# Performance work log

Measured on AMD Instinct MI355X. Metric: run time of the kernel, lower is better.

The kernel has to match this reference:

```python
import jax, jax.numpy as jnp
import numpy as np

N_NODES = 50000
N_EDGES = 200000
N_GRAPH = 1024
H = 128          # hidden_channels
POS = 48         # pos_offset
NF = 256         # num_filters in SchNetInteraction
L = 5            # n_layers
NFF = 512
MAX_ITEM = 300


def ssp(v):
    # shifted softplus used by SchNet
    return jax.nn.softplus(v) - jnp.log(2.0)


def setup_inputs() -> dict:
    key = jax.random.key(0)
    ks = iter(jax.random.split(key, 40))
    s = 0.05
    inp = {}
    inp['x'] = jax.random.randint(next(ks), (N_NODES,), 0, MAX_ITEM)
    inp['edge_index'] = jax.random.randint(next(ks), (2, N_EDGES), 0, N_NODES)
    inp['edge_attr'] = jax.random.normal(next(ks), (N_EDGES, 4), jnp.float32)
    inp['batch'] = jnp.sort(jax.random.randint(next(ks), (N_NODES,), 0, N_GRAPH))
    inp['pos'] = jax.random.normal(next(ks), (N_NODES, 3), jnp.float32)
    # embedding / projection params
    vert = jax.random.normal(next(ks), (MAX_ITEM + 1, H - POS), jnp.float32) * s
    inp['vert_emb'] = vert.at[MAX_ITEM].set(0.0)  # padding_idx
    inp['pos_w'] = jax.random.normal(next(ks), (POS, 3), jnp.float32) * s
    inp['edge_w'] = jax.random.normal(next(ks), (H, 4), jnp.float32) * s
    # per-layer SchNetInteraction params (stacked over L)
    inp['filt_w1'] = jax.random.normal(next(ks), (L, NF, H), jnp.float32) * s
    inp['filt_b1'] = jnp.zeros((L, NF), jnp.float32)
    inp['filt_w2'] = jax.random.normal(next(ks), (L, NF, NF), jnp.float32) * s
    inp['filt_b2'] = jnp.zeros((L, NF), jnp.float32)
    inp['lin1_w'] = jax.random.normal(next(ks), (L, NF, H), jnp.float32) * s
    inp['lin2_w'] = jax.random.normal(next(ks), (L, H, NF), jnp.float32) * s
    inp['lin2_b'] = jnp.zeros((L, H), jnp.float32)
    inp['lin3_w'] = jax.random.normal(next(ks), (L, H, H), jnp.float32) * s
    inp['lin3_b'] = jnp.zeros((L, H), jnp.float32)
    # per-layer edge MLP: Linear(edge_ch + in_ch -> in_ch) + Tanh
    inp['em_w'] = jax.random.normal(next(ks), (L, H, 2 * H), jnp.float32) * s
    inp['em_b'] = jnp.zeros((L, H), jnp.float32)
    # head
    inp['head_w1'] = jax.random.normal(next(ks), (NFF, H), jnp.float32) * s
    inp['head_b1'] = jnp.zeros((NFF,), jnp.float32)
    inp['head_w2'] = jax.random.normal(next(ks), (1, NFF), jnp.float32) * s
    inp['head_b2'] = jnp.zeros((1,), jnp.float32)
    return inp


def _forward(x, edge_index, edge_attr, batch, pos, vert_emb, pos_w, edge_w,
             filt_w1, filt_b1, filt_w2, filt_b2, lin1_w, lin2_w, lin2_b,
             lin3_w, lin3_b, em_w, em_b, head_w1, head_b1, head_w2, head_b2):
    n = x.shape[0]
    src, dst = edge_index[0], edge_index[1]
    h = jnp.concatenate([vert_emb[x], pos @ pos_w.T], axis=-1)  # [N, H]
    ea = edge_attr @ edge_w.T                                    # [E, H]
    for i in range(L):
        # SchNetInteraction / CFConv: per-edge filter MLP, gather, scatter-sum
        W = ssp(ea @ filt_w1[i].T + filt_b1[i]) @ filt_w2[i].T + filt_b2[i]  # [E, NF]
        hj = (h @ lin1_w[i].T)[src]                                          # [E, NF]
        agg = jax.ops.segment_sum(hj * W, dst, num_segments=n)               # [N, NF]
        out = ssp(agg @ lin2_w[i].T + lin2_b[i]) @ lin3_w[i].T + lin3_b[i]   # [N, H]
        h = jax.nn.relu(out) + h  # relu + residual skip
        # edge MLP update (always active in ResGraphModule)
        ea = jnp.tanh(jnp.concatenate([ea, h[src] + h[dst]], axis=-1) @ em_w[i].T + em_b[i]) + ea
    # global mean pool over graphs
    ssum = jax.ops.segment_sum(h, batch, num_segments=N_GRAPH)               # [G, H]
    cnt = jax.ops.segment_sum(jnp.ones((n,), h.dtype), batch, num_segments=N_GRAPH)
    g = ssum / jnp.maximum(cnt, 1.0)[:, None]
    # head: Linear -> GELU (exact, as torch default) -> Dropout(eval) -> Linear
    y = jax.nn.gelu(g @ head_w1.T + head_b1, approximate=False) @ head_w2.T + head_b2
    return y  # [G, 1]


def reference(x, edge_index, edge_attr, batch, pos, vert_emb, pos_w, edge_w,
              filt_w1, filt_b1, filt_w2, filt_b2, lin1_w, lin2_w, lin2_b,
              lin3_w, lin3_b, em_w, em_b, head_w1, head_b1, head_w2, head_b2):
    return _forward(x, edge_index, edge_attr, batch, pos, vert_emb, pos_w, edge_w,
                    filt_w1, filt_b1, filt_w2, filt_b2, lin1_w, lin2_w, lin2_b,
                    lin3_w, lin3_b, em_w, em_b, head_w1, head_b1, head_w2, head_b2)
```

## Files before the change

### kernel.cpp

```cpp
#include <hip/hip_runtime.h>
#include <hip/hip_bf16.h>
#include <math.h>

#define N_NODES 50000
#define N_EDGES 200000
#define N_GRAPH 1024
#define HC      128
#define NFC     256
#define NLAYER  5
#define NFFC    512

typedef short bf16x8 __attribute__((ext_vector_type(8)));
typedef float f4v    __attribute__((ext_vector_type(4)));

__device__ __forceinline__ float ssp_f(float x) {
  float e = __expf(-fabsf(x));
  return fmaxf(x, 0.0f) + __logf(1.0f + e) - 0.69314718055994530942f;
}
__device__ __forceinline__ float tanh_f(float x) {
  float e = __expf(2.0f * fabsf(x));
  float t = 1.0f - 2.0f * __builtin_amdgcn_rcpf(e + 1.0f);
  return copysignf(t, x);
}
__device__ __forceinline__ unsigned short f2bf(float x) {
  union { float f; unsigned u; } v; v.f = x;
  unsigned r = v.u + 0x7fff + ((v.u >> 16) & 1);
  return (unsigned short)(r >> 16);
}
__device__ __forceinline__ float bf2f(unsigned short b) {
  union { unsigned u; float f; } v; v.u = (unsigned)b << 16; return v.f;
}

__global__ void zero_kernel(float4* __restrict__ p, int n4) {
  int i = blockIdx.x * blockDim.x + threadIdx.x;
  if (i < n4) p[i] = make_float4(0.f, 0.f, 0.f, 0.f);
}
__global__ void zeroi_kernel(int* __restrict__ p, int n) {
  int i = blockIdx.x * blockDim.x + threadIdx.x;
  if (i < n) p[i] = 0;
}

__global__ void hist_kernel(const int* __restrict__ ei, int* __restrict__ deg) {
  int e = blockIdx.x * blockDim.x + threadIdx.x;
  if (e < N_EDGES) atomicAdd(&deg[ei[N_EDGES + e]], 1);
}
__global__ void scan1_kernel(const int* __restrict__ deg, int* __restrict__ excl,
                             int* __restrict__ bsum, int n) {
  __shared__ int buf[256];
  const int tid = threadIdx.x;
  const int i = blockIdx.x * 256 + tid;
  int v = (i < n) ? deg[i] : 0;
  buf[tid] = v;
  __syncthreads();
  for (int s = 1; s < 256; s <<= 1) {
    int t = (tid >= s) ? buf[tid - s] : 0;
    __syncthreads();
    buf[tid] += t;
    __syncthreads();
  }
  if (i < n) excl[i] = buf[tid] - v;
  if (tid == 255) bsum[blockIdx.x] = buf[255];
}
__global__ void scan2_kernel(int* __restrict__ bsum, int nb) {
// ... 37 lines not shown

__global__ void wconv_kernel(const float* __restrict__ w,
                             unsigned short* __restrict__ hi, int n) {
  int i = blockIdx.x * blockDim.x + threadIdx.x;
  if (i < n) hi[i] = f2bf(w[i]);
}

__global__ void embed_kernel(const int* __restrict__ x, const float* __restrict__ pos,
                             const float* __restrict__ vert, const float* __restrict__ posw,
                             unsigned short* __restrict__ h) {
  int n = blockIdx.x;
  int c = threadIdx.x;
  float v;
  if (c < 80) {
    v = vert[(size_t)x[n] * 80 + c];
  } else {
    int j = c - 80;
    v = pos[n*3+0]*posw[j*3+0] + pos[n*3+1]*posw[j*3+1] + pos[n*3+2]*posw[j*3+2];
  }
  h[(size_t)n*HC + c] = f2bf(v);
}

__global__ void edgeproj_kernel(const float* __restrict__ eattr, const float* __restrict__ ew,
                                unsigned short* __restrict__ eaP,
                                const int* __restrict__ ipos) {
  int idx = blockIdx.x * blockDim.x + threadIdx.x;
  if (idx >= N_EDGES * HC) return;
  int e = idx >> 7, c = idx & 127;
  const float* a = eattr + (size_t)e*4;
  const float* w = ew + (size_t)c*4;
  eaP[(size_t)ipos[e]*HC + c] = f2bf(a[0]*w[0] + a[1]*w[1] + a[2]*w[2] + a[3]*w[3]);
}

__global__ __launch_bounds__(256, 4) void emlite_kernel(
    unsigned short* eaP,
    const unsigned short* __restrict__ Bh,
    const float* __restrict__ bias,
    const int* __restrict__ eiPs, const int* __restrict__ eiPd,
    const unsigned short* __restrict__ hfeat)
{
  __shared__ unsigned short ldsA[64][136];
  __shared__ unsigned short ldsH[64][136];

  const int tid  = threadIdx.x;
  const int m0   = blockIdx.x * 64;
  const int lane = tid & 63, wave = tid >> 6;
  const int quad = lane >> 4, l16 = lane & 15;
  const int r = tid >> 2, cb = (tid & 3) * 32;

  const int e = m0 + r;
  const int s = eiPs[e], d = eiPd[e];

  {
    const unsigned short* ap = eaP + (size_t)e * HC + cb;
#pragma unroll
    for (int q = 0; q < 4; q++)
      *(bf16x8*)&ldsA[r][cb + q*8] = *(const bf16x8*)(ap + q*8);
    const unsigned short* p1 = hfeat + (size_t)s * HC + cb;
    const unsigned short* p2 = hfeat + (size_t)d * HC + cb;
    unsigned short x1[32], x2[32], th[32];
#pragma unroll
    for (int q = 0; q < 4; q++) {
      *(bf16x8*)&x1[q*8] = *(const bf16x8*)(p1 + q*8);
      *(bf16x8*)&x2[q*8] = *(const bf16x8*)(p2 + q*8);
    }
#pragma unroll
    for (int j = 0; j < 32; j++) th[j] = f2bf(bf2f(x1[j]) + bf2f(x2[j]));
#pragma unroll
    for (int q = 0; q < 4; q++)
      *(bf16x8*)&ldsH[r][cb + q*8] = *(bf16x8*)&th[q*8];
  }

  const f4v zf = {0.f, 0.f, 0.f, 0.f};
  f4v acc[4][2];
#pragma unroll
  for (int mt = 0; mt < 4; mt++) { acc[mt][0] = zf; acc[mt][1] = zf; }

  __syncthreads();

#pragma unroll
  for (int nt = 0; nt < 2; nt++) {
    const size_t brow = (size_t)(wave*32 + nt*16 + l16);
#pragma unroll
    for (int kk = 0; kk < 128; kk += 32) {
      bf16x8 b = *(const bf16x8*)&Bh[brow * 2*HC + kk + quad*8];
#pragma unroll
      for (int mt = 0; mt < 4; mt++) {
        bf16x8 a = *(const bf16x8*)&ldsA[mt*16 + l16][kk + quad*8];
        acc[mt][nt] = __builtin_amdgcn_mfma_f32_16x16x32_bf16(a, b, acc[mt][nt], 0, 0, 0);
      }
    }
#pragma unroll
    for (int kk = 0; kk < 128; kk += 32) {
      bf16x8 b = *(const bf16x8*)&Bh[brow * 2*HC + HC + kk + quad*8];
#pragma unroll
      for (int mt = 0; mt < 4; mt++) {
        bf16x8 a = *(const bf16x8*)&ldsH[mt*16 + l16][kk + quad*8];
        acc[mt][nt] = __builtin_amdgcn_mfma_f32_16x16x32_bf16(a, b, acc[mt][nt], 0, 0, 0);
      }
    }
  }

#pragma unroll
  for (int nt = 0; nt < 2; nt++) {
    const int col = wave*32 + nt*16 + l16;
    const float bz = bias[col];
#pragma unroll
    for (int mt = 0; mt < 4; mt++) {
      const int rowb = mt*16 + quad*4;
#pragma unroll
      for (int rr = 0; rr < 4; rr++) {
        const size_t idx = (size_t)(m0 + rowb + rr) * HC + col;
        eaP[idx] = f2bf(tanh_f(acc[mt][nt][rr] + bz) + bf2f(ldsA[rowb + rr][col]));
      }
    }
  }
}

__global__ __launch_bounds__(256, 2) void nodeup_kernel(
    float* __restrict__ agg,
    const unsigned short* __restrict__ L2h,
    const float* __restrict__ b2,
    const unsigned short* __restrict__ L3h,
    const float* __restrict__ b3,
    unsigned short* h)
{
  __shared__ unsigned short lds[128 * 136];

  const int tid  = threadIdx.x;
  const int m0   = blockIdx.x * 128;
  const int lane = tid & 63, wave = tid >> 6;
  const int quad = lane >> 4, l16 = lane & 15;
  const int wm = (wave >> 1) * 64, wn = (wave & 1) * 64;
  const int r  = tid >> 1;
  const int c0 = (tid & 1) * 16;

  const f4v zf = {0.f, 0.f, 0.f, 0.f};
  f4v acc[4][4];
#pragma unroll
  for (int i = 0; i < 4; i++)
#pragma unroll
    for (int j = 0; j < 4; j++) acc[i][j] = zf;

  const bool mok = (m0 + r) < N_NODES;
  const size_t arow = (size_t)(m0 + r);

  float av[16];
  if (mok) {
    const float* ap = agg + arow * NFC + c0;
#pragma unroll
    for (int q = 0; q < 4; q++) *(float4*)&av[q*4] = *(const float4*)(ap + q*4);
  } else {
#pragma unroll
    for (int j = 0; j < 16; j++) av[j] = 0.f;
  }

  for (int kk = 0; kk < NFC; kk += 32) {
    float avn[16];
    if (kk + 32 < NFC) {
      if (mok) {
        const float* ap = agg + arow * NFC + kk + 32 + c0;
#pragma unroll
        for (int q = 0; q < 4; q++) *(float4*)&avn[q*4] = *(const float4*)(ap + q*4);
      } else {
#pragma unroll
        for (int j = 0; j < 16; j++) avn[j] = 0.f;
      }
    }
    bf16x8 b[4];
#pragma unroll
    for (int nt = 0; nt < 4; nt++) {
      const size_t brow = (size_t)(wn + nt*16 + l16);
      b[nt] = *(const bf16x8*)&L2h[brow * NFC + kk + quad*8];
    }
    __syncthreads();
    unsigned short th[16];
#pragma unroll
    for (int j = 0; j < 16; j++) th[j] = f2bf(av[j]);
    *(bf16x8*)&lds[r*40 + c0]     = *(bf16x8*)&th[0];
    *(bf16x8*)&lds[r*40 + c0 + 8] = *(bf16x8*)&th[8];
    __syncthreads();
    bf16x8 a[4];
#pragma unroll
    for (int t = 0; t < 4; t++)
      a[t] = *(const bf16x8*)&lds[(wm + t*16 + l16) * 40 + quad * 8];
#pragma unroll
    for (int mt = 0; mt < 4; mt++)
#pragma unroll
      for (int nt = 0; nt < 4; nt++)
        acc[mt][nt] = __builtin_amdgcn_mfma_f32_16x16x32_bf16(a[mt], b[nt], acc[mt][nt], 0, 0, 0);
    if (kk + 32 < NFC) {
#pragma unroll
      for (int j = 0; j < 16; j++) av[j] = avn[j];
    }
  }
  __syncthreads();

  if (mok) {
    float4* zp = (float4*)(agg + arow * NFC + (tid & 1) * 128);
    const float4 z4 = make_float4(0.f, 0.f, 0.f, 0.f);
#pragma unroll
    for (int q = 0; q < 32; q++) zp[q] = z4;
  }

#pragma unroll
  for (int nt = 0; nt < 4; nt++) {
    const int col = wn + nt*16 + l16;
    const float bz = b2[col];
#pragma unroll
    for (int mt = 0; mt < 4; mt++) {
      const int rowb = wm + mt*16 + quad*4;
#pragma unroll
      for (int rr = 0; rr < 4; rr++)
        lds[(rowb+rr)*136 + col] = f2bf(ssp_f(acc[mt][nt][rr] + bz));
    }
  }
  __syncthreads();

  f4v acc2[4][4];
#pragma unroll
  for (int i = 0; i < 4; i++)
#pragma unroll
    for (int j = 0; j < 4; j++) acc2[i][j] = zf;

  for (int kk = 0; kk < HC; kk += 32) {
    bf16x8 b[4];
#pragma unroll
    for (int nt = 0; nt < 4; nt++) {
      const size_t brow = (size_t)(wn + nt*16 + l16);
      b[nt] = *(const bf16x8*)&L3h[brow * HC + kk + quad*8];
    }
    bf16x8 a[4];
#pragma unroll
    for (int t = 0; t < 4; t++)
      a[t] = *(const bf16x8*)&lds[(wm + t*16 + l16) * 136 + kk + quad * 8];
#pragma unroll
    for (int mt = 0; mt < 4; mt++)
#pragma unroll
      for (int nt = 0; nt < 4; nt++)
        acc2[mt][nt] = __builtin_amdgcn_mfma_f32_16x16x32_bf16(a[mt], b[nt], acc2[mt][nt], 0, 0, 0);
  }

#pragma unroll
  for (int nt = 0; nt < 4; nt++) {
    const int ncol = wn + nt*16 + l16;
    const float bz = b3[ncol];
#pragma unroll
    for (int mt = 0; mt < 4; mt++) {
      const int mb = wm + mt*16 + quad*4;
#pragma unroll
      for (int rr = 0; rr < 4; rr++) {
        const int m = m0 + mb + rr;
        if (m < N_NODES) {
          const size_t idx = (size_t)m * HC + ncol;
          h[idx] = f2bf(fmaxf(acc2[mt][nt][rr] + bz, 0.f) + bf2f(h[idx]));
        }
      }
    }
  }
}

__device__ __forceinline__ int sigma_row(int r) {
  return ((r >> 2) & 3) * 16 + (r >> 4) * 4 + (r & 3);
}
__global__ __launch_bounds__(256, 3) void ffs_kernel(
    const unsigned short* __restrict__ eaP,
    const unsigned short* __restrict__ l1h,
    const unsigned short* __restrict__ fw1h,
    const float* __restrict__ fb1,
    const unsigned short* __restrict__ fw2h,
    const float* __restrict__ fb2,
    const int* __restrict__ eiPs, const int* __restrict__ eiPd,
    const unsigned short* __restrict__ hfeat, float* __restrict__ agg)
{
  __shared__ unsigned short ldsA[64][136];
  __shared__ unsigned short ldsB[64][136];
  __shared__ int sD[64];

  const int tid  = threadIdx.x;
  const int m0   = blockIdx.x * 64;
  const int lane = tid & 63, wave = tid >> 6;
  const int quad = lane >> 4, l16 = lane & 15;
  const int r = tid >> 2, cb = (tid & 3) * 32;
  const int sp = m0 + sigma_row(r);

  const int s = eiPs[sp];
  bf16x8 hreg[4];
  {
    const unsigned short* hp = hfeat + (size_t)s * HC + cb;
#pragma unroll
    for (int q = 0; q < 4; q++) hreg[q] = *(const bf16x8*)(hp + q*8);
  }
  if (tid < 64) sD[tid] = eiPd[m0 + sigma_row(tid)];

  {
    const unsigned short* ap = eaP + (size_t)sp * HC + cb;
#pragma unroll
    for (int q = 0; q < 4; q++)
      *(bf16x8*)&ldsA[r][cb + q*8] = *(const bf16x8*)(ap + q*8);
  }

  const f4v zf = {0.f, 0.f, 0.f, 0.f};
  f4v wacc[4][4];
#pragma unroll
  for (int mt = 0; mt < 4; mt++)
#pragma unroll
    for (int nt = 0; nt < 4; nt++) wacc[mt][nt] = zf;

  __syncthreads();

  for (int p = 0; p < 4; p++) {
    f4v tacc[4];
#pragma unroll
    for (int mt = 0; mt < 4; mt++) tacc[mt] = zf;
    const size_t b1row = (size_t)(p*64 + wave*16 + l16);
#pragma unroll
    for (int kk = 0; kk < 128; kk += 32) {
      bf16x8 b = *(const bf16x8*)&fw1h[b1row * HC + kk + quad*8];
#pragma unroll
      for (int mt = 0; mt < 4; mt++) {
        bf16x8 a = *(const bf16x8*)&ldsA[mt*16 + l16][kk + quad*8];
        tacc[mt] = __builtin_amdgcn_mfma_f32_16x16x32_bf16(a, b, tacc[mt], 0, 0, 0);
      }
    }
    {
      const int col = wave*16 + l16;
      const float bz = fb1[p*64 + col];
#pragma unroll
      for (int mt = 0; mt < 4; mt++) {
        const int rowb = mt*16 + quad*4;
#pragma unroll
        for (int rr = 0; rr < 4; rr++)
          ldsB[rowb+rr][col] = f2bf(ssp_f(tacc[mt][rr] + bz));
      }
    }
    __syncthreads();

#pragma unroll
    for (int kc = 0; kc < 2; kc++) {
      bf16x8 a_[4];
#pragma unroll
      for (int mt = 0; mt < 4; mt++)
        a_[mt] = *(const bf16x8*)&ldsB[mt*16 + l16][kc*32 + quad*8];
#pragma unroll
      for (int nt = 0; nt < 4; nt++) {
        const size_t brow = (size_t)(wave*64 + nt*16 + l16);
        bf16x8 b = *(const bf16x8*)&fw2h[brow * NFC + p*64 + kc*32 + quad*8];
#pragma unroll
        for (int mt = 0; mt < 4; mt++)
          wacc[mt][nt] = __builtin_amdgcn_mfma_f32_16x16x32_bf16(a_[mt], b, wacc[mt][nt], 0, 0, 0);
      }
    }
    __syncthreads();
  }

#pragma unroll
  for (int q = 0; q < 4; q++)
    *(bf16x8*)&ldsB[r][cb + q*8] = hreg[q];
  __syncthreads();

  f4v hacc[4][4];
#pragma unroll
  for (int mt = 0; mt < 4; mt++)
#pragma unroll
    for (int nt = 0; nt < 4; nt++) hacc[mt][nt] = zf;

#pragma unroll
  for (int kk = 0; kk < 128; kk += 32) {
    bf16x8 a_[4];
#pragma unroll
    for (int mt = 0; mt < 4; mt++)
      a_[mt] = *(const bf16x8*)&ldsB[mt*16 + l16][kk + quad*8];
#pragma unroll
    for (int nt = 0; nt < 4; nt++) {
      const size_t brow = (size_t)(wave*64 + nt*16 + l16);
      bf16x8 b = *(const bf16x8*)&l1h[brow * HC + kk + quad*8];
#pragma unroll
      for (int mt = 0; mt < 4; mt++)
        hacc[mt][nt] = __builtin_amdgcn_mfma_f32_16x16x32_bf16(a_[mt], b, hacc[mt][nt], 0, 0, 0);
    }
  }

#pragma unroll
  for (int nt = 0; nt < 4; nt++) {
    const int col = wave*64 + nt*16 + l16;
    const float bz = fb2[col];
    float accum = 0.f;
    int prev = -1;
    bool firstrun = true;
#pragma unroll
    for (int mt = 0; mt < 4; mt++) {
#pragma unroll
      for (int rr = 0; rr < 4; rr++) {
        const int prow = mt*16 + quad*4 + rr;
        const int d = sD[prow];
        const float v = (wacc[mt][nt][rr] + bz) * hacc[mt][nt][rr];
        if (d != prev) {
          if (prev >= 0) {
            if (firstrun) atomicAdd(&agg[(size_t)prev * NFC + col], accum);
            else          agg[(size_t)prev * NFC + col] = accum;
            firstrun = false;
          }
          accum = v; prev = d;
        } else {
          accum += v;
        }
      }
    }
    atomicAdd(&agg[(size_t)prev * NFC + col], accum);
  }
}

__global__ __launch_bounds__(256) void poolhead_kernel(
    const int* __restrict__ batch, const unsigned short* __restrict__ h,
    const float* __restrict__ w1, const float* __restrict__ b1,
    const float* __restrict__ w2, const float* __restrict__ b2,
    float* __restrict__ y)
{
  __shared__ float gs[HC];
  __shared__ float red[256];
  const int g = blockIdx.x;
  const int tid = threadIdx.x;

  int lo = 0, hi = N_NODES;
  while (lo < hi) { int m = (lo + hi) >> 1; if (batch[m] < g) lo = m + 1; else hi = m; }
  int lo2 = lo, hi2 = N_NODES;
  while (lo2 < hi2) { int m = (lo2 + hi2) >> 1; if (batch[m] < g + 1) lo2 = m + 1; else hi2 = m; }
  const int cnt = lo2 - lo;

  if (tid < HC) {
    float s = 0.f;
    for (int i = lo; i < lo2; i++) s += bf2f(h[(size_t)i * HC + tid]);
    gs[tid] = s / (float)max(cnt, 1);
  }
  __syncthreads();

  float partial = 0.f;
  for (int f = tid; f < NFFC; f += 256) {
    float acc = b1[f];
    const float* wr = w1 + (size_t)f * HC;
#pragma unroll 8
    for (int k = 0; k < HC; k++) acc = fmaf(gs[k], wr[k], acc);
// ... 56 lines not shown
  unsigned short* fw2h = (unsigned short*)alloc((size_t)n_fw2*2);
  unsigned short* l1h  = (unsigned short*)alloc((size_t)n_l1*2);
  unsigned short* l2h  = (unsigned short*)alloc((size_t)n_l2*2);
  unsigned short* l3h  = (unsigned short*)alloc((size_t)n_l3*2);
  unsigned short* emh  = (unsigned short*)alloc((size_t)n_em*2);

  const int NSCAN = N_NODES + 1;
  const int NB    = (NSCAN + 255) / 256;

  zeroi_kernel<<<(NSCAN+255)/256, 256, 0, stream>>>(deg, NSCAN);
  hist_kernel<<<(N_EDGES+255)/256, 256, 0, stream>>>(ei, deg);
  scan1_kernel<<<NB, 256, 0, stream>>>(deg, cursor, bsum, NSCAN);
  scan2_kernel<<<1, 256, 0, stream>>>(bsum, NB);
  scan3_kernel<<<NB, 256, 0, stream>>>(cursor, bsum, NSCAN);
  perm_kernel<<<(N_EDGES+255)/256, 256, 0, stream>>>(ei, cursor, perm);
  eperm_kernel<<<(N_EDGES+255)/256, 256, 0, stream>>>(ei, perm, eiPs, eiPd, ipos);

  wconv_kernel<<<(n_fw1+255)/256, 256, 0, stream>>>(fw1, fw1h, n_fw1);
  wconv_kernel<<<(n_fw2+255)/256, 256, 0, stream>>>(fw2, fw2h, n_fw2);
  wconv_kernel<<<(n_l1 +255)/256, 256, 0, stream>>>(l1w, l1h, n_l1);
  wconv_kernel<<<(n_l2 +255)/256, 256, 0, stream>>>(l2w, l2h, n_l2);
  wconv_kernel<<<(n_l3 +255)/256, 256, 0, stream>>>(l3w, l3h, n_l3);
  wconv_kernel<<<(n_em +255)/256, 256, 0, stream>>>(emw, emh, n_em);

  const int GN   = (N_NODES + 127) / 128;
  const int GE64 = N_EDGES / 64;

  embed_kernel<<<N_NODES, 128, 0, stream>>>(x, pos, vert, posw, h);
  edgeproj_kernel<<<(N_EDGES*HC + 255)/256, 256, 0, stream>>>(eattr, edgew, eaP, ipos);
  zero_kernel<<<((N_NODES*NFC/4) + 255)/256, 256, 0, stream>>>(
      (float4*)agg, N_NODES*NFC/4);

  for (int i = 0; i < NLAYER; ++i) {
    ffs_kernel<<<GE64, 256, 0, stream>>>(
        eaP, l1h + (size_t)i*NFC*HC,
        fw1h + (size_t)i*NFC*HC, fb1 + (size_t)i*NFC,
        fw2h + (size_t)i*NFC*NFC, fb2 + (size_t)i*NFC,
        eiPs, eiPd, h, agg);
    nodeup_kernel<<<GN, 256, 0, stream>>>(
        agg, l2h + (size_t)i*HC*NFC, l2b + (size_t)i*HC,
        l3h + (size_t)i*HC*HC, l3b + (size_t)i*HC, h);
    if (i < NLAYER - 1) {
      emlite_kernel<<<GE64, 256, 0, stream>>>(
          eaP, emh + (size_t)i*HC*2*HC, emb + (size_t)i*HC,
          eiPs, eiPd, h);
    }
  }

  poolhead_kernel<<<N_GRAPH, 256, 0, stream>>>(batch, h, hw1, hb1, hw2, hb2, out);
}
```

Before: 1.492 ms.

## Fuse edge-MLP update into filter kernel and double-buffer filter stages

Folds the per-layer edge MLP (tanh update of edge features) into the start of the next layer's filter/message kernel, reusing the already-loaded edge tile and source-node features so the edge features stay in shared memory rather than taking an extra global round trip and launch. The filter network's two-stage loop is unrolled with double-buffered LDS tiles, which removes one barrier per stage and overlaps the next first-layer GEMM with the second-layer consume. The node-update kernel now converts the whole aggregate row to bf16 in LDS up front instead of streaming it in chunks with two barriers per step. This costs more LDS and register pressure in the fused kernel and adds a runtime branch for the first layer.

```diff
diff --git a/kernel.cpp b/kernel.cpp
--- a/kernel.cpp
+++ b/kernel.cpp
@@ -132,249 +132,70 @@
   eaP[(size_t)ipos[e]*HC + c] = f2bf(a[0]*w[0] + a[1]*w[1] + a[2]*w[2] + a[3]*w[3]);
 }
 
-__global__ __launch_bounds__(256, 4) void emlite_kernel(
+__device__ __forceinline__ int sigma_row(int r) {
+  return ((r >> 2) & 3) * 16 + (r >> 4) * 4 + (r & 3);
+}
+
+#define TACC_COMPUTE(TDST, P)                                                   \
+  {                                                                             \
+    _Pragma("unroll")                                                           \
+    for (int mt_ = 0; mt_ < 4; mt_++) TDST[mt_] = zf;                           \
+    const size_t b1row_ = (size_t)((P)*64 + wave*16 + l16);                     \
+    _Pragma("unroll")                                                           \
+    for (int kk_ = 0; kk_ < 128; kk_ += 32) {                                   \
+      bf16x8 b_ = *(const bf16x8*)&fw1h[b1row_ * HC + kk_ + quad*8];            \
+      _Pragma("unroll")                                                         \
+      for (int mt_ = 0; mt_ < 4; mt_++) {                                       \
+        bf16x8 a_ = *(const bf16x8*)&ldsA[mt_*16 + l16][kk_ + quad*8];          \
+        TDST[mt_] = __builtin_amdgcn_mfma_f32_16x16x32_bf16(a_, b_, TDST[mt_], 0, 0, 0); \
+      }                                                                         \
+    }                                                                           \
+  }
+
+#define TWRITE(TSRC, BUF, P)                                                    \
+  {                                                                             \
+    const int col_ = wave*16 + l16;                                             \
+    const float bz_ = fb1[(P)*64 + col_];                                       \
+    _Pragma("unroll")                                                           \
+    for (int mt_ = 0; mt_ < 4; mt_++) {                                         \
+      const int rowb_ = mt_*16 + quad*4;                                        \
+      _Pragma("unroll")                                                         \
+      for (int rr_ = 0; rr_ < 4; rr_++)                                         \
+        ldsT[BUF][rowb_+rr_][col_] = f2bf(ssp_f(TSRC[mt_][rr_] + bz_));         \
+    }                                                                           \
+  }
+
+#define WCONSUME(BUF, P)                                                        \
+  {                                                                             \
+    _Pragma("unroll")                                                           \
+    for (int kc_ = 0; kc_ < 2; kc_++) {                                         \
+      bf16x8 av_[4];                                                            \
+      _Pragma("unroll")                                                         \
+      for (int mt_ = 0; mt_ < 4; mt_++)                                         \
+        av_[mt_] = *(const bf16x8*)&ldsT[BUF][mt_*16 + l16][kc_*32 + quad*8];   \
+      _Pragma("unroll")                                                         \
+      for (int nt_ = 0; nt_ < 4; nt_++) {                                       \
+        const size_t brow_ = (size_t)(wave*64 + nt_*16 + l16);                  \
+        bf16x8 b_ = *(const bf16x8*)&fw2h[brow_ * NFC + (P)*64 + kc_*32 + quad*8]; \
+        _Pragma("unroll")                                                       \
+        for (int mt_ = 0; mt_ < 4; mt_++)                                       \
+          wacc[mt_][nt_] = __builtin_amdgcn_mfma_f32_16x16x32_bf16(av_[mt_], b_, wacc[mt_][nt_], 0, 0, 0); \
+      }                                                                         \
+    }                                                                           \
+  }
+
+__global__ __launch_bounds__(256, 3) void emffs_kernel(
     unsigned short* eaP,
-    const unsigned short* __restrict__ Bh,
-    const float* __restrict__ bias,
+    const unsigned short* __restrict__ emWh, const float* __restrict__ emB,
+    const unsigned short* __restrict__ l1h,
+    const unsigned short* __restrict__ fw1h, const float* __restrict__ fb1,
+    const unsigned short* __restrict__ fw2h, const float* __restrict__ fb2,
     const int* __restrict__ eiPs, const int* __restrict__ eiPd,
-    const unsigned short* __restrict__ hfeat)
+    const unsigned short* __restrict__ hfeat, float* __restrict__ agg,
+    const int do_em)
 {
   __shared__ unsigned short ldsA[64][136];
-  __shared__ unsigned short ldsH[64][136];
-
-  const int tid  = threadIdx.x;
-  const int m0   = blockIdx.x * 64;
-  const int lane = tid & 63, wave = tid >> 6;
-  const int quad = lane >> 4, l16 = lane & 15;
-  const int r = tid >> 2, cb = (tid & 3) * 32;
-
-  const int e = m0 + r;
-  const int s = eiPs[e], d = eiPd[e];
-
-  {
-    const unsigned short* ap = eaP + (size_t)e * HC + cb;
-#pragma unroll
-    for (int q = 0; q < 4; q++)
-      *(bf16x8*)&ldsA[r][cb + q*8] = *(const bf16x8*)(ap + q*8);
-    const unsigned short* p1 = hfeat + (size_t)s * HC + cb;
-    const unsigned short* p2 = hfeat + (size_t)d * HC + cb;
-    unsigned short x1[32], x2[32], th[32];
-#pragma unroll
-    for (int q = 0; q < 4; q++) {
-      *(bf16x8*)&x1[q*8] = *(const bf16x8*)(p1 + q*8);
-      *(bf16x8*)&x2[q*8] = *(const bf16x8*)(p2 + q*8);
-    }
-#pragma unroll
-    for (int j = 0; j < 32; j++) th[j] = f2bf(bf2f(x1[j]) + bf2f(x2[j]));
-#pragma unroll
-    for (int q = 0; q < 4; q++)
-      *(bf16x8*)&ldsH[r][cb + q*8] = *(bf16x8*)&th[q*8];
-  }
-
-  const f4v zf = {0.f, 0.f, 0.f, 0.f};
-  f4v acc[4][2];
-#pragma unroll
-  for (int mt = 0; mt < 4; mt++) { acc[mt][0] = zf; acc[mt][1] = zf; }
-
-  __syncthreads();
-
-#pragma unroll
-  for (int nt = 0; nt < 2; nt++) {
-    const size_t brow = (size_t)(wave*32 + nt*16 + l16);
-#pragma unroll
-    for (int kk = 0; kk < 128; kk += 32) {
-      bf16x8 b = *(const bf16x8*)&Bh[brow * 2*HC + kk + quad*8];
-#pragma unroll
-      for (int mt = 0; mt < 4; mt++) {
-        bf16x8 a = *(const bf16x8*)&ldsA[mt*16 + l16][kk + quad*8];
-        acc[mt][nt] = __builtin_amdgcn_mfma_f32_16x16x32_bf16(a, b, acc[mt][nt], 0, 0, 0);
-      }
-    }
-#pragma unroll
-    for (int kk = 0; kk < 128; kk += 32) {
-      bf16x8 b = *(const bf16x8*)&Bh[brow * 2*HC + HC + kk + quad*8];
-#pragma unroll
-      for (int mt = 0; mt < 4; mt++) {
-        bf16x8 a = *(const bf16x8*)&ldsH[mt*16 + l16][kk + quad*8];
-        acc[mt][nt] = __builtin_amdgcn_mfma_f32_16x16x32_bf16(a, b, acc[mt][nt], 0, 0, 0);
-      }
-    }
-  }
-
-#pragma unroll
-  for (int nt = 0; nt < 2; nt++) {
-    const int col = wave*32 + nt*16 + l16;
-    const float bz = bias[col];
-#pragma unroll
-    for (int mt = 0; mt < 4; mt++) {
-      const int rowb = mt*16 + quad*4;
-#pragma unroll
-      for (int rr = 0; rr < 4; rr++) {
-        const size_t idx = (size_t)(m0 + rowb + rr) * HC + col;
-        eaP[idx] = f2bf(tanh_f(acc[mt][nt][rr] + bz) + bf2f(ldsA[rowb + rr][col]));
-      }
-    }
-  }
-}
-
-__global__ __launch_bounds__(256, 2) void nodeup_kernel(
-    float* __restrict__ agg,
-    const unsigned short* __restrict__ L2h,
-    const float* __restrict__ b2,
-    const unsigned short* __restrict__ L3h,
-    const float* __restrict__ b3,
-    unsigned short* h)
-{
-  __shared__ unsigned short lds[128 * 136];
-
-  const int tid  = threadIdx.x;
-  const int m0   = blockIdx.x * 128;
-  const int lane = tid & 63, wave = tid >> 6;
-  const int quad = lane >> 4, l16 = lane & 15;
-  const int wm = (wave >> 1) * 64, wn = (wave & 1) * 64;
-  const int r  = tid >> 1;
-  const int c0 = (tid & 1) * 16;
-
-  const f4v zf = {0.f, 0.f, 0.f, 0.f};
-  f4v acc[4][4];
-#pragma unroll
-  for (int i = 0; i < 4; i++)
-#pragma unroll
-    for (int j = 0; j < 4; j++) acc[i][j] = zf;
-
-  const bool mok = (m0 + r) < N_NODES;
-  const size_t arow = (size_t)(m0 + r);
-
-  float av[16];
-  if (mok) {
-    const float* ap = agg + arow * NFC + c0;
-#pragma unroll
-    for (int q = 0; q < 4; q++) *(float4*)&av[q*4] = *(const float4*)(ap + q*4);
-  } else {
-#pragma unroll
-    for (int j = 0; j < 16; j++) av[j] = 0.f;
-  }
-
-  for (int kk = 0; kk < NFC; kk += 32) {
-    float avn[16];
-    if (kk + 32 < NFC) {
-      if (mok) {
-        const float* ap = agg + arow * NFC + kk + 32 + c0;
-#pragma unroll
-        for (int q = 0; q < 4; q++) *(float4*)&avn[q*4] = *(const float4*)(ap + q*4);
-      } else {
-#pragma unroll
-        for (int j = 0; j < 16; j++) avn[j] = 0.f;
-      }
-    }
-    bf16x8 b[4];
-#pragma unroll
-    for (int nt = 0; nt < 4; nt++) {
-      const size_t brow = (size_t)(wn + nt*16 + l16);
-      b[nt] = *(const bf16x8*)&L2h[brow * NFC + kk + quad*8];
-    }
-    __syncthreads();
-    unsigned short th[16];
-#pragma unroll
-    for (int j = 0; j < 16; j++) th[j] = f2bf(av[j]);
-    *(bf16x8*)&lds[r*40 + c0]     = *(bf16x8*)&th[0];
-    *(bf16x8*)&lds[r*40 + c0 + 8] = *(bf16x8*)&th[8];
-    __syncthreads();
-    bf16x8 a[4];
-#pragma unroll
-    for (int t = 0; t < 4; t++)
-      a[t] = *(const bf16x8*)&lds[(wm + t*16 + l16) * 40 + quad * 8];
-#pragma unroll
-    for (int mt = 0; mt < 4; mt++)
-#pragma unroll
-      for (int nt = 0; nt < 4; nt++)
-        acc[mt][nt] = __builtin_amdgcn_mfma_f32_16x16x32_bf16(a[mt], b[nt], acc[mt][nt], 0, 0, 0);
-    if (kk + 32 < NFC) {
-#pragma unroll
-      for (int j = 0; j < 16; j++) av[j] = avn[j];
-    }
-  }
-  __syncthreads();
-
-  if (mok) {
-    float4* zp = (float4*)(agg + arow * NFC + (tid & 1) * 128);
-    const float4 z4 = make_float4(0.f, 0.f, 0.f, 0.f);
-#pragma unroll
-    for (int q = 0; q < 32; q++) zp[q] = z4;
-  }
-
-#pragma unroll
-  for (int nt = 0; nt < 4; nt++) {
-    const int col = wn + nt*16 + l16;
-    const float bz = b2[col];
-#pragma unroll
-    for (int mt = 0; mt < 4; mt++) {
-      const int rowb = wm + mt*16 + quad*4;
-#pragma unroll
-      for (int rr = 0; rr < 4; rr++)
-        lds[(rowb+rr)*136 + col] = f2bf(ssp_f(acc[mt][nt][rr] + bz));
-    }
-  }
-  __syncthreads();
-
-  f4v acc2[4][4];
-#pragma unroll
-  for (int i = 0; i < 4; i++)
-#pragma unroll
-    for (int j = 0; j < 4; j++) acc2[i][j] = zf;
-
-  for (int kk = 0; kk < HC; kk += 32) {
-    bf16x8 b[4];
-#pragma unroll
-    for (int nt = 0; nt < 4; nt++) {
-      const size_t brow = (size_t)(wn + nt*16 + l16);
-      b[nt] = *(const bf16x8*)&L3h[brow * HC + kk + quad*8];
-    }
-    bf16x8 a[4];
-#pragma unroll
-    for (int t = 0; t < 4; t++)
-      a[t] = *(const bf16x8*)&lds[(wm + t*16 + l16) * 136 + kk + quad * 8];
-#pragma unroll
-    for (int mt = 0; mt < 4; mt++)
-#pragma unroll
-      for (int nt = 0; nt < 4; nt++)
-        acc2[mt][nt] = __builtin_amdgcn_mfma_f32_16x16x32_bf16(a[mt], b[nt], acc2[mt][nt], 0, 0, 0);
-  }
-
-#pragma unroll
-  for (int nt = 0; nt < 4; nt++) {
-    const int ncol = wn + nt*16 + l16;
-    const float bz = b3[ncol];
-#pragma unroll
-    for (int mt = 0; mt < 4; mt++) {
-      const int mb = wm + mt*16 + quad*4;
-#pragma unroll
-      for (int rr = 0; rr < 4; rr++) {
-        const int m = m0 + mb + rr;
-        if (m < N_NODES) {
-          const size_t idx = (size_t)m * HC + ncol;
-          h[idx] = f2bf(fmaxf(acc2[mt][nt][rr] + bz, 0.f) + bf2f(h[idx]));
-        }
-      }
-    }
-  }
-}
-
-__device__ __forceinline__ int sigma_row(int r) {
-  return ((r >> 2) & 3) * 16 + (r >> 4) * 4 + (r & 3);
-}
-__global__ __launch_bounds__(256, 3) void ffs_kernel(
-    const unsigned short* __restrict__ eaP,
-    const unsigned short* __restrict__ l1h,
-    const unsigned short* __restrict__ fw1h,
-    const float* __restrict__ fb1,
-    const unsigned short* __restrict__ fw2h,
-    const float* __restrict__ fb2,
-    const int* __restrict__ eiPs, const int* __restrict__ eiPd,
-    const unsigned short* __restrict__ hfeat, float* __restrict__ agg)
-{
-  __shared__ unsigned short ldsA[64][136];
-  __shared__ unsigned short ldsB[64][136];
+  __shared__ unsigned short ldsT[2][64][72];
   __shared__ int sD[64];
 
   const int tid  = threadIdx.x;
@@ -400,63 +221,104 @@
       *(bf16x8*)&ldsA[r][cb + q*8] = *(const bf16x8*)(ap + q*8);
   }
 
+  unsigned short* ldsH = &ldsT[0][0][0];
+  if (do_em) {
+    const int d = eiPd[sp];
+    const unsigned short* dp = hfeat + (size_t)d * HC + cb;
+    unsigned short th[32];
+#pragma unroll
+    for (int q = 0; q < 4; q++) {
+      bf16x8 x2 = *(const bf16x8*)(dp + q*8);
+#pragma unroll
+      for (int j = 0; j < 8; j++) {
+        unsigned short a16 = ((const unsigned short*)&hreg[q])[j];
+        unsigned short b16 = ((const unsigned short*)&x2)[j];
+        th[q*8 + j] = f2bf(bf2f(a16) + bf2f(b16));
+      }
+    }
+#pragma unroll
+    for (int q = 0; q < 4; q++)
+      *(bf16x8*)&ldsH[r*136 + cb + q*8] = *(bf16x8*)&th[q*8];
+  }
+
   const f4v zf = {0.f, 0.f, 0.f, 0.f};
-  f4v wacc[4][4];
-#pragma unroll
-  for (int mt = 0; mt < 4; mt++)
-#pragma unroll
-    for (int nt = 0; nt < 4; nt++) wacc[mt][nt] = zf;
-
-  __syncthreads();
-
-  for (int p = 0; p < 4; p++) {
-    f4v tacc[4];
-#pragma unroll
-    for (int mt = 0; mt < 4; mt++) tacc[mt] = zf;
-    const size_t b1row = (size_t)(p*64 + wave*16 + l16);
-#pragma unroll
-    for (int kk = 0; kk < 128; kk += 32) {
-      bf16x8 b = *(const bf16x8*)&fw1h[b1row * HC + kk + quad*8];
-#pragma unroll
-      for (int mt = 0; mt < 4; mt++) {
-        bf16x8 a = *(const bf16x8*)&ldsA[mt*16 + l16][kk + quad*8];
-        tacc[mt] = __builtin_amdgcn_mfma_f32_16x16x32_bf16(a, b, tacc[mt], 0, 0, 0);
+  __syncthreads();
+
+  if (do_em) {
+    f4v acc[4][2];
+#pragma unroll
+    for (int mt = 0; mt < 4; mt++) { acc[mt][0] = zf; acc[mt][1] = zf; }
+#pragma unroll
+    for (int nt = 0; nt < 2; nt++) {
+      const size_t brow = (size_t)(wave*32 + nt*16 + l16);
+#pragma unroll
+      for (int kk = 0; kk < 128; kk += 32) {
+        bf16x8 b = *(const bf16x8*)&emWh[brow * 2*HC + kk + quad*8];
+#pragma unroll
+        for (int mt = 0; mt < 4; mt++) {
+          bf16x8 a = *(const bf16x8*)&ldsA[mt*16 + l16][kk + quad*8];
+          acc[mt][nt] = __builtin_amdgcn_mfma_f32_16x16x32_bf16(a, b, acc[mt][nt], 0, 0, 0);
+        }
       }
-    }
-    {
-      const int col = wave*16 + l16;
-      const float bz = fb1[p*64 + col];
+#pragma unroll
+      for (int kk = 0; kk < 128; kk += 32) {
+        bf16x8 b = *(const bf16x8*)&emWh[brow * 2*HC + HC + kk + quad*8];
+#pragma unroll
+        for (int mt = 0; mt < 4; mt++) {
+          bf16x8 a = *(const bf16x8*)&ldsH[(mt*16 + l16)*136 + kk + quad*8];
+          acc[mt][nt] = __builtin_amdgcn_mfma_f32_16x16x32_bf16(a, b, acc[mt][nt], 0, 0, 0);
+        }
+      }
+    }
+#pragma unroll
+    for (int nt = 0; nt < 2; nt++) {
+      const int col = wave*32 + nt*16 + l16;
+      const float bz = emB[col];
 #pragma unroll
       for (int mt = 0; mt < 4; mt++) {
         const int rowb = mt*16 + quad*4;
 #pragma unroll
-        for (int rr = 0; rr < 4; rr++)
-          ldsB[rowb+rr][col] = f2bf(ssp_f(tacc[mt][rr] + bz));
+        for (int rr = 0; rr < 4; rr++) {
+          const int row = rowb + rr;
+          ldsA[row][col] = f2bf(tanh_f(acc[mt][nt][rr] + bz) + bf2f(ldsA[row][col]));
+        }
       }
     }
     __syncthreads();
-
-#pragma unroll
-    for (int kc = 0; kc < 2; kc++) {
-      bf16x8 a_[4];
-#pragma unroll
-      for (int mt = 0; mt < 4; mt++)
-        a_[mt] = *(const bf16x8*)&ldsB[mt*16 + l16][kc*32 + quad*8];
-#pragma unroll
-      for (int nt = 0; nt < 4; nt++) {
-        const size_t brow = (size_t)(wave*64 + nt*16 + l16);
-        bf16x8 b = *(const bf16x8*)&fw2h[brow * NFC + p*64 + kc*32 + quad*8];
-#pragma unroll
-        for (int mt = 0; mt < 4; mt++)
-          wacc[mt][nt] = __builtin_amdgcn_mfma_f32_16x16x32_bf16(a_[mt], b, wacc[mt][nt], 0, 0, 0);
-      }
-    }
-    __syncthreads();
-  }
-
+    {
+      unsigned short* op = eaP + (size_t)sp * HC + cb;
+#pragma unroll
+      for (int q = 0; q < 4; q++)
+        *(bf16x8*)(op + q*8) = *(const bf16x8*)&ldsA[r][cb + q*8];
+    }
+  }
+
+  f4v wacc[4][4];
+#pragma unroll
+  for (int mt = 0; mt < 4; mt++)
+#pragma unroll
+    for (int nt = 0; nt < 4; nt++) wacc[mt][nt] = zf;
+
+  f4v t0[4], t1[4];
+  TACC_COMPUTE(t0, 0)
+  TWRITE(t0, 0, 0)
+  __syncthreads();
+  TACC_COMPUTE(t1, 1)
+  WCONSUME(0, 0)
+  TWRITE(t1, 1, 1)
+  __syncthreads();
+  TACC_COMPUTE(t0, 2)
+  WCONSUME(1, 1)
+  TWRITE(t0, 0, 2)
+  __syncthreads();
+  TACC_COMPUTE(t1, 3)
+  WCONSUME(0, 2)
+  TWRITE(t1, 1, 3)
+  __syncthreads();
+  WCONSUME(1, 3)
 #pragma unroll
   for (int q = 0; q < 4; q++)
-    *(bf16x8*)&ldsB[r][cb + q*8] = hreg[q];
+    *(bf16x8*)&ldsA[r][cb + q*8] = hreg[q];
   __syncthreads();
 
   f4v hacc[4][4];
@@ -470,7 +332,7 @@
     bf16x8 a_[4];
 #pragma unroll
     for (int mt = 0; mt < 4; mt++)
-      a_[mt] = *(const bf16x8*)&ldsB[mt*16 + l16][kk + quad*8];
+      a_[mt] = *(const bf16x8*)&ldsA[mt*16 + l16][kk + quad*8];
 #pragma unroll
     for (int nt = 0; nt < 4; nt++) {
       const size_t brow = (size_t)(wave*64 + nt*16 + l16);
@@ -508,6 +370,132 @@
       }
     }
     atomicAdd(&agg[(size_t)prev * NFC + col], accum);
+  }
+}
+
+__global__ __launch_bounds__(256, 2) void nodeup_kernel(
+    float* __restrict__ agg,
+    const unsigned short* __restrict__ L2h,
+    const float* __restrict__ b2,
+    const unsigned short* __restrict__ L3h,
+    const float* __restrict__ b3,
+    unsigned short* h)
+{
+  __shared__ unsigned short ldsS[128 * 264];
+
+  const int tid  = threadIdx.x;
+  const int m0   = blockIdx.x * 128;
+  const int lane = tid & 63, wave = tid >> 6;
+  const int quad = lane >> 4, l16 = lane & 15;
+  const int wm = (wave >> 1) * 64, wn = (wave & 1) * 64;
+  const int r  = tid >> 1;
+  const int ch = (tid & 1) * 128;
+
+  const bool mok = (m0 + r) < N_NODES;
+
+  if (mok) {
+    const float* ap = agg + (size_t)(m0 + r) * NFC + ch;
+#pragma unroll
+    for (int g = 0; g < 16; g++) {
+      float4 v0 = *(const float4*)(ap + g*8);
+      float4 v1 = *(const float4*)(ap + g*8 + 4);
+      unsigned short th[8];
+      th[0] = f2bf(v0.x); th[1] = f2bf(v0.y); th[2] = f2bf(v0.z); th[3] = f2bf(v0.w);
+      th[4] = f2bf(v1.x); th[5] = f2bf(v1.y); th[6] = f2bf(v1.z); th[7] = f2bf(v1.w);
+      *(bf16x8*)&ldsS[r*264 + ch + g*8] = *(bf16x8*)th;
+    }
+    float4* zp = (float4*)(agg + (size_t)(m0 + r) * NFC + ch);
+    const float4 z4 = make_float4(0.f, 0.f, 0.f, 0.f);
+#pragma unroll
+    for (int g = 0; g < 32; g++) zp[g] = z4;
+  } else {
+    const bf16x8 zb = {0, 0, 0, 0, 0, 0, 0, 0};
+#pragma unroll
+    for (int g = 0; g < 16; g++) *(bf16x8*)&ldsS[r*264 + ch + g*8] = zb;
+  }
+
+  const f4v zf = {0.f, 0.f, 0.f, 0.f};
+  f4v acc[4][4];
+#pragma unroll
+  for (int i = 0; i < 4; i++)
+#pragma unroll
+    for (int j = 0; j < 4; j++) acc[i][j] = zf;
+
+  __syncthreads();
+
+  for (int kk = 0; kk < NFC; kk += 32) {
+    bf16x8 b[4];
+#pragma unroll
+    for (int nt = 0; nt < 4; nt++) {
+      const size_t brow = (size_t)(wn + nt*16 + l16);
+      b[nt] = *(const bf16x8*)&L2h[brow * NFC + kk + quad*8];
+    }
+    bf16x8 a[4];
+#pragma unroll
+    for (int t = 0; t < 4; t++)
+      a[t] = *(const bf16x8*)&ldsS[(wm + t*16 + l16) * 264 + kk + quad*8];
+#pragma unroll
+    for (int mt = 0; mt < 4; mt++)
+#pragma unroll
+      for (int nt = 0; nt < 4; nt++)
+        acc[mt][nt] = __builtin_amdgcn_mfma_f32_16x16x32_bf16(a[mt], b[nt], acc[mt][nt], 0, 0, 0);
+  }
+  __syncthreads();
+
+#pragma unroll
+  for (int nt = 0; nt < 4; nt++) {
+    const int col = wn + nt*16 + l16;
+    const float bz = b2[col];
+#pragma unroll
+    for (int mt = 0; mt < 4; mt++) {
+      const int rowb = wm + mt*16 + quad*4;
+#pragma unroll
+      for (int rr = 0; rr < 4; rr++)
+        ldsS[(rowb+rr)*136 + col] = f2bf(ssp_f(acc[mt][nt][rr] + bz));
+    }
+  }
+  __syncthreads();
+
+  f4v acc2[4][4];
+#pragma unroll
+  for (int i = 0; i < 4; i++)
+#pragma unroll
+    for (int j = 0; j < 4; j++) acc2[i][j] = zf;
+
+  for (int kk = 0; kk < HC; kk += 32) {
+    bf16x8 b[4];
+#pragma unroll
+    for (int nt = 0; nt < 4; nt++) {
+      const size_t brow = (size_t)(wn + nt*16 + l16);
+      b[nt] = *(const bf16x8*)&L3h[brow * HC + kk + quad*8];
+    }
+    bf16x8 a[4];
+#pragma unroll
+    for (int t = 0; t < 4; t++)
+      a[t] = *(const bf16x8*)&ldsS[(wm + t*16 + l16) * 136 + kk + quad * 8];
+#pragma unroll
+    for (int mt = 0; mt < 4; mt++)
+#pragma unroll
+      for (int nt = 0; nt < 4; nt++)
+        acc2[mt][nt] = __builtin_amdgcn_mfma_f32_16x16x32_bf16(a[mt], b[nt], acc2[mt][nt], 0, 0, 0);
+  }
+
+#pragma unroll
+  for (int nt = 0; nt < 4; nt++) {
+    const int ncol = wn + nt*16 + l16;
+    const float bz = b3[ncol];
+#pragma unroll
+    for (int mt = 0; mt < 4; mt++) {
+      const int mb = wm + mt*16 + quad*4;
+#pragma unroll
+      for (int rr = 0; rr < 4; rr++) {
+        const int m = m0 + mb + rr;
+        if (m < N_NODES) {
+          const size_t idx = (size_t)m * HC + ncol;
+          h[idx] = f2bf(fmaxf(acc2[mt][nt][rr] + bz, 0.f) + bf2f(h[idx]));
+        }
+      }
+    }
   }
 }
 
@@ -630,19 +618,17 @@
       (float4*)agg, N_NODES*NFC/4);
 
   for (int i = 0; i < NLAYER; ++i) {
-    ffs_kernel<<<GE64, 256, 0, stream>>>(
-        eaP, l1h + (size_t)i*NFC*HC,
+    const int em_i = (i > 0) ? (i - 1) : 0;
+    emffs_kernel<<<GE64, 256, 0, stream>>>(
+        eaP,
+        emh + (size_t)em_i*HC*2*HC, emb + (size_t)em_i*HC,
+        l1h + (size_t)i*NFC*HC,
         fw1h + (size_t)i*NFC*HC, fb1 + (size_t)i*NFC,
         fw2h + (size_t)i*NFC*NFC, fb2 + (size_t)i*NFC,
-        eiPs, eiPd, h, agg);
+        eiPs, eiPd, h, agg, (i > 0) ? 1 : 0);
     nodeup_kernel<<<GN, 256, 0, stream>>>(
         agg, l2h + (size_t)i*HC*NFC, l2b + (size_t)i*HC,
         l3h + (size_t)i*HC*HC, l3b + (size_t)i*HC, h);
-    if (i < NLAYER - 1) {
-      emlite_kernel<<<GE64, 256, 0, stream>>>(
-          eaP, emh + (size_t)i*HC*2*HC, emb + (size_t)i*HC,
-          eiPs, eiPd, h);
-    }
   }
 
   poolhead_kernel<<<N_GRAPH, 256, 0, stream>>>(batch, h, hw1, hb1, hw2, hb2, out);
```

Result: slower. 1.522 ms (+2.0%).

## Swizzle LDS tiles and restructure filter and node-update staging to cut barriers

Applied to the files above, without the earlier changes.

Replaces padded LDS arrays with XOR-swizzled layouts in the edge MLP, node update and filter kernels. The node update kernel now converts the whole agg row tile to bf16 in LDS once and zeroes agg up front, which removes the per-k-step double barrier. The filter kernel computes all four filter chunks into a full 64x256 LDS buffer before the second GEMM, replacing per-chunk barriers with one, and raises wave priority around the MFMA loop. LDS use grows (64KB in nodeup, about 48KB in the filter kernel), which may lower occupancy.

```diff
diff --git a/kernel.cpp b/kernel.cpp
--- a/kernel.cpp
+++ b/kernel.cpp
@@ -29,6 +29,13 @@
 }
 __device__ __forceinline__ float bf2f(unsigned short b) {
   union { unsigned u; float f; } v; v.u = (unsigned)b << 16; return v.f;
+}
+
+__device__ __forceinline__ int swzA(int row, int col) {
+  return (row << 7) + (((col >> 3) ^ (row & 7)) << 3) + (col & 7);
+}
+__device__ __forceinline__ int swzT(int row, int col) {
+  return (row << 8) + (((col >> 3) ^ (row & 7)) << 3) + (col & 7);
 }
 
 __global__ void zero_kernel(float4* __restrict__ p, int n4) {
@@ -139,8 +146,8 @@
     const int* __restrict__ eiPs, const int* __restrict__ eiPd,
     const unsigned short* __restrict__ hfeat)
 {
-  __shared__ unsigned short ldsA[64][136];
-  __shared__ unsigned short ldsH[64][136];
+  __shared__ unsigned short ldsA[64 * 128];
+  __shared__ unsigned short ldsH[64 * 128];
 
   const int tid  = threadIdx.x;
   const int m0   = blockIdx.x * 64;
@@ -155,7 +162,7 @@
     const unsigned short* ap = eaP + (size_t)e * HC + cb;
 #pragma unroll
     for (int q = 0; q < 4; q++)
-      *(bf16x8*)&ldsA[r][cb + q*8] = *(const bf16x8*)(ap + q*8);
+      *(bf16x8*)&ldsA[swzA(r, cb + q*8)] = *(const bf16x8*)(ap + q*8);
     const unsigned short* p1 = hfeat + (size_t)s * HC + cb;
     const unsigned short* p2 = hfeat + (size_t)d * HC + cb;
     unsigned short x1[32], x2[32], th[32];
@@ -168,7 +175,7 @@
     for (int j = 0; j < 32; j++) th[j] = f2bf(bf2f(x1[j]) + bf2f(x2[j]));
 #pragma unroll
     for (int q = 0; q < 4; q++)
-      *(bf16x8*)&ldsH[r][cb + q*8] = *(bf16x8*)&th[q*8];
+      *(bf16x8*)&ldsH[swzA(r, cb + q*8)] = *(bf16x8*)&th[q*8];
   }
 
   const f4v zf = {0.f, 0.f, 0.f, 0.f};
@@ -186,7 +193,7 @@
       bf16x8 b = *(const bf16x8*)&Bh[brow * 2*HC + kk + quad*8];
 #pragma unroll
       for (int mt = 0; mt < 4; mt++) {
-        bf16x8 a = *(const bf16x8*)&ldsA[mt*16 + l16][kk + quad*8];
+        bf16x8 a = *(const bf16x8*)&ldsA[swzA(mt*16 + l16, kk + quad*8)];
         acc[mt][nt] = __builtin_amdgcn_mfma_f32_16x16x32_bf16(a, b, acc[mt][nt], 0, 0, 0);
       }
     }
@@ -195,7 +202,7 @@
       bf16x8 b = *(const bf16x8*)&Bh[brow * 2*HC + HC + kk + quad*8];
 #pragma unroll
       for (int mt = 0; mt < 4; mt++) {
-        bf16x8 a = *(const bf16x8*)&ldsH[mt*16 + l16][kk + quad*8];
+        bf16x8 a = *(const bf16x8*)&ldsH[swzA(mt*16 + l16, kk + quad*8)];
         acc[mt][nt] = __builtin_amdgcn_mfma_f32_16x16x32_bf16(a, b, acc[mt][nt], 0, 0, 0);
       }
     }
@@ -211,7 +218,7 @@
 #pragma unroll
       for (int rr = 0; rr < 4; rr++) {
         const size_t idx = (size_t)(m0 + rowb + rr) * HC + col;
-        eaP[idx] = f2bf(tanh_f(acc[mt][nt][rr] + bz) + bf2f(ldsA[rowb + rr][col]));
+        eaP[idx] = f2bf(tanh_f(acc[mt][nt][rr] + bz) + bf2f(ldsA[swzA(rowb + rr, col)]));
       }
     }
   }
@@ -225,7 +232,7 @@
     const float* __restrict__ b3,
     unsigned short* h)
 {
-  __shared__ unsigned short lds[128 * 136];
+  __shared__ unsigned short ldsS[128 * 256];
 
   const int tid  = threadIdx.x;
   const int m0   = blockIdx.x * 128;
@@ -233,7 +240,30 @@
   const int quad = lane >> 4, l16 = lane & 15;
   const int wm = (wave >> 1) * 64, wn = (wave & 1) * 64;
   const int r  = tid >> 1;
-  const int c0 = (tid & 1) * 16;
+  const int ch = (tid & 1) * 128;
+
+  const bool mok = (m0 + r) < N_NODES;
+
+  if (mok) {
+    const float* ap = agg + (size_t)(m0 + r) * NFC + ch;
+#pragma unroll
+    for (int g = 0; g < 16; g++) {
+      float4 v0 = *(const float4*)(ap + g*8);
+      float4 v1 = *(const float4*)(ap + g*8 + 4);
+      unsigned short th[8];
+      th[0] = f2bf(v0.x); th[1] = f2bf(v0.y); th[2] = f2bf(v0.z); th[3] = f2bf(v0.w);
+      th[4] = f2bf(v1.x); th[5] = f2bf(v1.y); th[6] = f2bf(v1.z); th[7] = f2bf(v1.w);
+      *(bf16x8*)&ldsS[swzT(r, ch + g*8)] = *(bf16x8*)th;
+    }
+    float4* zp = (float4*)(agg + (size_t)(m0 + r) * NFC + ch);
+    const float4 z4 = make_float4(0.f, 0.f, 0.f, 0.f);
+#pragma unroll
+    for (int g = 0; g < 32; g++) zp[g] = z4;
+  } else {
+    const bf16x8 zb = {0, 0, 0, 0, 0, 0, 0, 0};
+#pragma unroll
+    for (int g = 0; g < 16; g++) *(bf16x8*)&ldsS[swzT(r, ch + g*8)] = zb;
+  }
 
   const f4v zf = {0.f, 0.f, 0.f, 0.f};
   f4v acc[4][4];
@@ -242,66 +272,26 @@
 #pragma unroll
     for (int j = 0; j < 4; j++) acc[i][j] = zf;
 
-  const bool mok = (m0 + r) < N_NODES;
-  const size_t arow = (size_t)(m0 + r);
-
-  float av[16];
-  if (mok) {
-    const float* ap = agg + arow * NFC + c0;
-#pragma unroll
-    for (int q = 0; q < 4; q++) *(float4*)&av[q*4] = *(const float4*)(ap + q*4);
-  } else {
-#pragma unroll
-    for (int j = 0; j < 16; j++) av[j] = 0.f;
-  }
+  __syncthreads();
 
   for (int kk = 0; kk < NFC; kk += 32) {
-    float avn[16];
-    if (kk + 32 < NFC) {
-      if (mok) {
-        const float* ap = agg + arow * NFC + kk + 32 + c0;
-#pragma unroll
-        for (int q = 0; q < 4; q++) *(float4*)&avn[q*4] = *(const float4*)(ap + q*4);
-      } else {
-#pragma unroll
-        for (int j = 0; j < 16; j++) avn[j] = 0.f;
-      }
-    }
     bf16x8 b[4];
 #pragma unroll
     for (int nt = 0; nt < 4; nt++) {
       const size_t brow = (size_t)(wn + nt*16 + l16);
       b[nt] = *(const bf16x8*)&L2h[brow * NFC + kk + quad*8];
     }
-    __syncthreads();
-    unsigned short th[16];
-#pragma unroll
-    for (int j = 0; j < 16; j++) th[j] = f2bf(av[j]);
-    *(bf16x8*)&lds[r*40 + c0]     = *(bf16x8*)&th[0];
-    *(bf16x8*)&lds[r*40 + c0 + 8] = *(bf16x8*)&th[8];
-    __syncthreads();
     bf16x8 a[4];
 #pragma unroll
     for (int t = 0; t < 4; t++)
-      a[t] = *(const bf16x8*)&lds[(wm + t*16 + l16) * 40 + quad * 8];
+      a[t] = *(const bf16x8*)&ldsS[swzT(wm + t*16 + l16, kk + quad*8)];
 #pragma unroll
     for (int mt = 0; mt < 4; mt++)
 #pragma unroll
       for (int nt = 0; nt < 4; nt++)
         acc[mt][nt] = __builtin_amdgcn_mfma_f32_16x16x32_bf16(a[mt], b[nt], acc[mt][nt], 0, 0, 0);
-    if (kk + 32 < NFC) {
-#pragma unroll
-      for (int j = 0; j < 16; j++) av[j] = avn[j];
-    }
-  }
-  __syncthreads();
-
-  if (mok) {
-    float4* zp = (float4*)(agg + arow * NFC + (tid & 1) * 128);
-    const float4 z4 = make_float4(0.f, 0.f, 0.f, 0.f);
-#pragma unroll
-    for (int q = 0; q < 32; q++) zp[q] = z4;
-  }
+  }
+  __syncthreads();
 
 #pragma unroll
   for (int nt = 0; nt < 4; nt++) {
@@ -312,7 +302,7 @@
       const int rowb = wm + mt*16 + quad*4;
 #pragma unroll
       for (int rr = 0; rr < 4; rr++)
-        lds[(rowb+rr)*136 + col] = f2bf(ssp_f(acc[mt][nt][rr] + bz));
+        ldsS[swzT(rowb+rr, col)] = f2bf(ssp_f(acc[mt][nt][rr] + bz));
     }
   }
   __syncthreads();
@@ -333,7 +323,7 @@
     bf16x8 a[4];
 #pragma unroll
     for (int t = 0; t < 4; t++)
-      a[t] = *(const bf16x8*)&lds[(wm + t*16 + l16) * 136 + kk + quad * 8];
+      a[t] = *(const bf16x8*)&ldsS[swzT(wm + t*16 + l16, kk + quad*8)];
 #pragma unroll
     for (int mt = 0; mt < 4; mt++)
 #pragma unroll
@@ -373,8 +363,8 @@
     const int* __restrict__ eiPs, const int* __restrict__ eiPd,
     const unsigned short* __restrict__ hfeat, float* __restrict__ agg)
 {
-  __shared__ unsigned short ldsA[64][136];
-  __shared__ unsigned short ldsB[64][136];
+  __shared__ unsigned short ldsA[64 * 128];
+  __shared__ unsigned short ldsT[64 * 256];
   __shared__ int sD[64];
 
   const int tid  = threadIdx.x;
@@ -397,16 +387,10 @@
     const unsigned short* ap = eaP + (size_t)sp * HC + cb;
 #pragma unroll
     for (int q = 0; q < 4; q++)
-      *(bf16x8*)&ldsA[r][cb + q*8] = *(const bf16x8*)(ap + q*8);
+      *(bf16x8*)&ldsA[swzA(r, cb + q*8)] = *(const bf16x8*)(ap + q*8);
   }
 
   const f4v zf = {0.f, 0.f, 0.f, 0.f};
-  f4v wacc[4][4];
-#pragma unroll
-  for (int mt = 0; mt < 4; mt++)
-#pragma unroll
-    for (int nt = 0; nt < 4; nt++) wacc[mt][nt] = zf;
-
   __syncthreads();
 
   for (int p = 0; p < 4; p++) {
@@ -419,29 +403,40 @@
       bf16x8 b = *(const bf16x8*)&fw1h[b1row * HC + kk + quad*8];
 #pragma unroll
       for (int mt = 0; mt < 4; mt++) {
-        bf16x8 a = *(const bf16x8*)&ldsA[mt*16 + l16][kk + quad*8];
+        bf16x8 a = *(const bf16x8*)&ldsA[swzA(mt*16 + l16, kk + quad*8)];
         tacc[mt] = __builtin_amdgcn_mfma_f32_16x16x32_bf16(a, b, tacc[mt], 0, 0, 0);
       }
     }
-    {
-      const int col = wave*16 + l16;
-      const float bz = fb1[p*64 + col];
-#pragma unroll
-      for (int mt = 0; mt < 4; mt++) {
-        const int rowb = mt*16 + quad*4;
-#pragma unroll
-        for (int rr = 0; rr < 4; rr++)
-          ldsB[rowb+rr][col] = f2bf(ssp_f(tacc[mt][rr] + bz));
-      }
-    }
-    __syncthreads();
-
+    const int col = p*64 + wave*16 + l16;
+    const float bz = fb1[col];
+#pragma unroll
+    for (int mt = 0; mt < 4; mt++) {
+      const int rowb = mt*16 + quad*4;
+#pragma unroll
+      for (int rr = 0; rr < 4; rr++)
+        ldsT[swzT(rowb+rr, col)] = f2bf(ssp_f(tacc[mt][rr] + bz));
+    }
+  }
+  __syncthreads();
+
+#pragma unroll
+  for (int q = 0; q < 4; q++)
+    *(bf16x8*)&ldsA[swzA(r, cb + q*8)] = hreg[q];
+
+  f4v wacc[4][4];
+#pragma unroll
+  for (int mt = 0; mt < 4; mt++)
+#pragma unroll
+    for (int nt = 0; nt < 4; nt++) wacc[mt][nt] = zf;
+
+  __builtin_amdgcn_s_setprio(1);
+  for (int p = 0; p < 4; p++) {
 #pragma unroll
     for (int kc = 0; kc < 2; kc++) {
       bf16x8 a_[4];
 #pragma unroll
       for (int mt = 0; mt < 4; mt++)
-        a_[mt] = *(const bf16x8*)&ldsB[mt*16 + l16][kc*32 + quad*8];
+        a_[mt] = *(const bf16x8*)&ldsT[swzT(mt*16 + l16, p*64 + kc*32 + quad*8)];
 #pragma unroll
       for (int nt = 0; nt < 4; nt++) {
         const size_t brow = (size_t)(wave*64 + nt*16 + l16);
@@ -451,12 +446,8 @@
           wacc[mt][nt] = __builtin_amdgcn_mfma_f32_16x16x32_bf16(a_[mt], b, wacc[mt][nt], 0, 0, 0);
       }
     }
-    __syncthreads();
-  }
-
-#pragma unroll
-  for (int q = 0; q < 4; q++)
-    *(bf16x8*)&ldsB[r][cb + q*8] = hreg[q];
+  }
+  __builtin_amdgcn_s_setprio(0);
   __syncthreads();
 
   f4v hacc[4][4];
@@ -470,7 +461,7 @@
     bf16x8 a_[4];
 #pragma unroll
     for (int mt = 0; mt < 4; mt++)
-      a_[mt] = *(const bf16x8*)&ldsB[mt*16 + l16][kk + quad*8];
+      a_[mt] = *(const bf16x8*)&ldsA[swzA(mt*16 + l16, kk + quad*8)];
 #pragma unroll
     for (int nt = 0; nt < 4; nt++) {
       const size_t brow = (size_t)(wave*64 + nt*16 + l16);
```

Result: no change. 1.485 ms (-0.5%).
